# Kernel tuning notes

Measured on AMD Instinct MI355X. Metric: run time of the kernel, lower is better.

The kernel has to match this reference:

```python
import jax, jax.numpy as jnp
import numpy as np

K = 4  # kNN neighbors


def build_edges(density_maps, k):
    B, _, H, W = density_maps.shape
    N = H * W
    flat = density_maps.reshape(B, N)
    # [B, N, N] pairwise absolute density distance
    dist = jnp.abs(flat[:, :, None] - flat[:, None, :])
    # k nearest (excluding self at position 0)
    tgt = jnp.argsort(dist, axis=2)[:, :, 1:k + 1]  # [B, N, k]
    src = jnp.broadcast_to(jnp.arange(N)[None, :, None], (B, N, k))
    offset = (jnp.arange(B) * N)[:, None, None]
    src = (src + offset).reshape(-1)
    tgt = (tgt + offset).reshape(-1)
    n_total = B * N
    loops = jnp.arange(n_total)
    row = jnp.concatenate([src, loops])  # source nodes
    col = jnp.concatenate([tgt, loops])  # target nodes
    return row, col, n_total


def gcn_conv(x, row, col, W, b, n_nodes):
    # symmetric deg^-1/2 normalization, deg computed on target (col)
    deg = jax.ops.segment_sum(jnp.ones_like(col, dtype=x.dtype), col, num_segments=n_nodes)
    dinv = jnp.where(deg > 0, jax.lax.rsqrt(deg), 0.0)
    norm = dinv[row] * dinv[col]  # [E]
    h = x @ W  # transform first, then propagate
    msg = norm[:, None] * h[row]
    out = jax.ops.segment_sum(msg, col, num_segments=n_nodes)
    return out + b


def setup_inputs() -> dict:
    key = jax.random.key(0)
    k1, k2, k3, k4, k5, k6 = jax.random.split(key, 6)
    B, Cin, Chid, Cout, H, W = 4, 256, 512, 256, 64, 64
    density_maps = jax.random.uniform(k1, (B, 1, H, W), dtype=jnp.float32)
    feature_maps = jax.random.normal(k2, (B, Cin, H, W), dtype=jnp.float32)
    W1 = jax.random.normal(k3, (Cin, Chid), dtype=jnp.float32) * (1.0 / np.sqrt(Cin))
    b1 = jnp.zeros((Chid,), dtype=jnp.float32)
    W2 = jax.random.normal(k4, (Chid, Cout), dtype=jnp.float32) * (1.0 / np.sqrt(Chid))
    b2 = jnp.zeros((Cout,), dtype=jnp.float32)
    return {"density_maps": density_maps, "feature_maps": feature_maps,
            "W1": W1, "b1": b1, "W2": W2, "b2": b2}


def reference(density_maps, feature_maps, W1, b1, W2, b2):
    B, Cin, H, Wd = feature_maps.shape
    row, col, n_total = build_edges(density_maps, K)
    # [B,C,H,W] -> [B*H*W, C] node features
    x = feature_maps.transpose(0, 2, 3, 1).reshape(-1, Cin)
    h = jax.nn.relu(gcn_conv(x, row, col, W1, b1, n_total))
    out = jax.nn.relu(gcn_conv(h, row, col, W2, b2, n_total))
    return out.reshape(B, H, Wd, -1).transpose(0, 3, 1, 2)
```

## Files before the change

kernel.cpp:

```cpp
#include <hip/hip_runtime.h>
#include <hip/hip_bf16.h>
#include <stdint.h>

#define N_NODES 16384
#define NPB     4096
#define NB      4
#define KNN     4
#define WIN     12
#define NBUK    4096

typedef short bf16x8 __attribute__((ext_vector_type(8)));
typedef float f32x4 __attribute__((ext_vector_type(4)));
typedef unsigned short u16x8 __attribute__((ext_vector_type(8)));

__device__ __forceinline__ unsigned short f2bf(float f) {
  unsigned u = __float_as_uint(f);
  unsigned r = (u + 0x7fff + ((u >> 16) & 1)) >> 16;
  return (unsigned short)r;
}
__device__ __forceinline__ float bf2f(unsigned short u) {
  return __uint_as_float(((unsigned)u) << 16);
}

__global__ __launch_bounds__(1024)
void bucket_kernel(const float* __restrict__ dm,
                   unsigned long long* __restrict__ skeys_g,
                   int* __restrict__ rank_g,
                   int* __restrict__ deg) {
  __shared__ int sHist[4096];
  __shared__ int sCur[4096];
  __shared__ unsigned long long sKeys[4096];
  int* part1 = (int*)sKeys;
  int* part2 = (int*)(sKeys + 512);
  const int t = threadIdx.x, b = blockIdx.x;
  const float* d = dm + b * NPB;

  unsigned long long kv[4]; int bk[4];
#pragma unroll
  for (int r = 0; r < 4; ++r) {
    int i = t + r * 1024;
    sHist[i] = 0;
    deg[b * NPB + i] = 1;
  }
  __syncthreads();
#pragma unroll
  for (int r = 0; r < 4; ++r) {
    int i = t + r * 1024;
    float v = d[i];
    kv[r] = (((unsigned long long)__float_as_uint(v)) << 32) | (unsigned)i;
    int k = (int)(v * (float)NBUK); if (k > NBUK - 1) k = NBUK - 1;
    bk[r] = k;
    atomicAdd(&sHist[k], 1);
  }
  __syncthreads();
  int c0 = sHist[4 * t + 0], c1 = sHist[4 * t + 1];
  int c2 = sHist[4 * t + 2], c3 = sHist[4 * t + 3];
  part1[t] = c0 + c1 + c2 + c3;
  __syncthreads();
  if (t < 64) {
    int s = 0;
#pragma unroll
    for (int k = 0; k < 16; ++k) s += part1[16 * t + k];
    part2[t] = s;
  }
  __syncthreads();
  if (t == 0) {
    int a = 0;
    for (int u = 0; u < 64; ++u) { int v = part2[u]; part2[u] = a; a += v; }
  }
  __syncthreads();
  int base = part2[t >> 4];
  for (int k = (t >> 4) * 16; k < t; ++k) base += part1[k];
  sHist[4 * t + 0] = base; sCur[4 * t + 0] = base; base += c0;
  sHist[4 * t + 1] = base; sCur[4 * t + 1] = base; base += c1;
  sHist[4 * t + 2] = base; sCur[4 * t + 2] = base; base += c2;
  sHist[4 * t + 3] = base; sCur[4 * t + 3] = base;
  __syncthreads();
#pragma unroll
  for (int r = 0; r < 4; ++r) {
    int slot = atomicAdd(&sCur[bk[r]], 1);
    sKeys[slot] = kv[r];
  }
  __syncthreads();
#pragma unroll
  for (int r = 0; r < 4; ++r) {
    int g = t + r * 1024;
    int s0 = sHist[g];
    int s1 = (g == NPB - 1) ? NPB : sHist[g + 1];
    for (int i = s0 + 1; i < s1; ++i) {
      unsigned long long x = sKeys[i];
      int j = i - 1;
      while (j >= s0 && sKeys[j] > x) { sKeys[j + 1] = sKeys[j]; --j; }
      sKeys[j + 1] = x;
    }
  }
  __syncthreads();
#pragma unroll
  for (int r = 0; r < 4; ++r) {
    int i = t + r * 1024;
    unsigned long long k = sKeys[i];
    skeys_g[b * NPB + i] = k;
    rank_g[b * NPB + (int)(k & 0xffffffffull)] = i;
  }
}

__global__ void knn_select_kernel(const unsigned long long* __restrict__ skeys,
                                  int* __restrict__ tgt, int* __restrict__ deg) {
  int p = blockIdx.x * 256 + threadIdx.x;
  if (p >= N_NODES) return;
  int b = p >> 12, pl = p & (NPB - 1);
  const unsigned long long* sk = skeys + b * NPB;
  unsigned long long kp = sk[pl];
  float di = __uint_as_float((unsigned)(kp >> 32));
  int lo = pl - WIN; if (lo < 0) lo = 0;
  int hi = pl + WIN; if (hi > NPB - 1) hi = NPB - 1;
  unsigned long long k0 = ~0ull, k1 = ~0ull, k2 = ~0ull, k3 = ~0ull, k4 = ~0ull;
  for (int q = lo; q <= hi; ++q) {
    unsigned long long key = sk[q];
    float v = __uint_as_float((unsigned)(key >> 32));
    float dist = fabsf(di - v);
    unsigned long long dk = (((unsigned long long)__float_as_uint(dist)) << 24) |
                            ((key & 0xfffull) << 12) | (unsigned)q;
    if (dk < k4) {
      if (dk < k0)      { k4 = k3; k3 = k2; k2 = k1; k1 = k0; k0 = dk; }
      else if (dk < k1) { k4 = k3; k3 = k2; k2 = k1; k1 = dk; }
      else if (dk < k2) { k4 = k3; k3 = k2; k2 = dk; }
      else if (dk < k3) { k4 = k3; k3 = dk; }
      else              { k4 = dk; }
    }
  }
  int base = b * NPB;
  int t0 = base + (int)(k1 & 0xfff);
  int t1 = base + (int)(k2 & 0xfff);
  int t2 = base + (int)(k3 & 0xfff);
  int t3 = base + (int)(k4 & 0xfff);
  tgt[p * KNN + 0] = t0; atomicAdd(&deg[t0], 1);
  tgt[p * KNN + 1] = t1; atomicAdd(&deg[t1], 1);
  tgt[p * KNN + 2] = t2; atomicAdd(&deg[t2], 1);
  tgt[p * KNN + 3] = t3; atomicAdd(&deg[t3], 1);
}

__global__ void cvt_all_kernel(const float* __restrict__ fm, unsigned short* __restrict__ px0,
                               const float* __restrict__ W1, unsigned short* __restrict__ W1t,
                               const float* __restrict__ W2, unsigned short* __restrict__ W2t,
                               const int* __restrict__ rank) {
  __shared__ float tile[64][33];
  int z = blockIdx.z;
  const float* in; unsigned short* outbase; int Rin, Cin, r0, c0;
  bool perm = false;
  if (z < NB) {
    in = fm + (size_t)z * 256 * 4096; outbase = px0 + (size_t)z * NPB * 256;
    Rin = 256; Cin = 4096; perm = true;
    c0 = blockIdx.x * 32; r0 = blockIdx.y * 64;
  } else {
    int id = blockIdx.y * 128 + blockIdx.x;
    if (id < 64)       { in = W1; outbase = W1t; Rin = 256; Cin = 512; c0 = (id & 15) * 32; r0 = (id >> 4) * 64; }
    else if (id < 128) { id -= 64; in = W2; outbase = W2t; Rin = 512; Cin = 256; c0 = (id & 7) * 32; r0 = (id >> 3) * 64; }
    else return;
  }
  int tx = threadIdx.x & 31, ty = threadIdx.x >> 5;
  const float* ip = in + (size_t)(r0 + ty) * Cin + c0 + tx;
#pragma unroll
  for (int i = 0; i < 8; ++i) tile[ty + 8 * i][tx] = ip[(size_t)(8 * i) * Cin];
  __syncthreads();
  int orow = threadIdx.x >> 3;
  int oseg = (threadIdx.x & 7) * 8;
  int outrow = c0 + orow;
  if (perm) outrow = rank[(size_t)z * NPB + outrow];
  unsigned short* op = outbase + (size_t)outrow * Rin + r0 + oseg;
  u16x8 o;
#pragma unroll
  for (int k = 0; k < 8; ++k) o[k] = f2bf(tile[oseg + k][orow]);
  *(u16x8*)op = o;
}

__global__ void transpose_kernel(const float* __restrict__ in, float* __restrict__ out,
                                 int Rin, int Cin) {
  __shared__ float tile[32][33];
  int c0 = blockIdx.x * 32, r0 = blockIdx.y * 32, b = blockIdx.z;
  int tx = threadIdx.x & 31, ty = threadIdx.x >> 5;
  const float* ip = in + ((size_t)b * Rin + r0) * Cin + c0;
#pragma unroll
  for (int i = 0; i < 32; i += 8) tile[ty + i][tx] = ip[(size_t)(ty + i) * Cin + tx];
  __syncthreads();
  float* op = out + ((size_t)b * Cin + c0) * Rin + r0;
#pragma unroll
  for (int i = 0; i < 32; i += 8) op[(size_t)(ty + i) * Rin + tx] = tile[tx][ty + i];
}

__global__ void prop_kernel(const unsigned short* __restrict__ in,
                            unsigned short* __restrict__ out,
                            const int* __restrict__ tgt, const int* __restrict__ deg) {
  int i = blockIdx.x * 8 + (threadIdx.x >> 5);
  int l = threadIdx.x & 31;
  int b0 = i & ~(NPB - 1);
  int lo = i - WIN; if (lo < b0) lo = b0;
  int hi = i + WIN; if (hi > b0 + NPB - 1) hi = b0 + NPB - 1;
  float a[8] = {};
  for (int q = lo; q <= hi; ++q) {
    int4 tq = *(const int4*)(tgt + q * 4);
    int c = (q == i) + (tq.x == i) + (tq.y == i) + (tq.z == i) + (tq.w == i);
    if (c) {
      float dj = (float)c * rsqrtf((float)deg[q]);
      u16x8 u = *(const u16x8*)(in + (size_t)q * 256 + l * 8);
#pragma unroll
      for (int k = 0; k < 8; ++k) a[k] = fmaf(dj, bf2f(u[k]), a[k]);
    }
  }
  float di = rsqrtf((float)deg[i]);
  u16x8 o;
#pragma unroll
  for (int k = 0; k < 8; ++k) o[k] = f2bf(a[k] * di);
  *(u16x8*)(out + (size_t)i * 256 + l * 8) = o;
}

__global__ void prop2_kernel(const unsigned short* __restrict__ in,
                             float* __restrict__ out,
                             const int* __restrict__ tgt, const int* __restrict__ deg,
                             const float* __restrict__ bias,
                             const unsigned long long* __restrict__ skeys) {
  int i = blockIdx.x * 8 + (threadIdx.x >> 5);
  int l = threadIdx.x & 31;
  int b0 = i & ~(NPB - 1);
  int lo = i - WIN; if (lo < b0) lo = b0;
  int hi = i + WIN; if (hi > b0 + NPB - 1) hi = b0 + NPB - 1;
  float a[8] = {};
  for (int q = lo; q <= hi; ++q) {
    int4 tq = *(const int4*)(tgt + q * 4);
    int c = (q == i) + (tq.x == i) + (tq.y == i) + (tq.z == i) + (tq.w == i);
    if (c) {
      float dj = (float)c * rsqrtf((float)deg[q]);
      u16x8 u = *(const u16x8*)(in + (size_t)q * 256 + l * 8);
#pragma unroll
      for (int k = 0; k < 8; ++k) a[k] = fmaf(dj, bf2f(u[k]), a[k]);
    }
  }
  float di = rsqrtf((float)deg[i]);
  int node = b0 + (int)(skeys[i] & 0xffffffffull);
  float4 o0, o1;
  o0.x = fmaxf(a[0] * di + bias[l * 8 + 0], 0.f);
  o0.y = fmaxf(a[1] * di + bias[l * 8 + 1], 0.f);
  o0.z = fmaxf(a[2] * di + bias[l * 8 + 2], 0.f);
  o0.w = fmaxf(a[3] * di + bias[l * 8 + 3], 0.f);
  o1.x = fmaxf(a[4] * di + bias[l * 8 + 4], 0.f);
  o1.y = fmaxf(a[5] * di + bias[l * 8 + 5], 0.f);
  o1.z = fmaxf(a[6] * di + bias[l * 8 + 6], 0.f);
  o1.w = fmaxf(a[7] * di + bias[l * 8 + 7], 0.f);
  *(float4*)(out + (size_t)node * 256 + l * 8) = o0;
  *(float4*)(out + (size_t)node * 256 + l * 8 + 4) = o1;
}

template <bool BIAS_RELU, bool OUT_BF16, int NI>
__global__ __launch_bounds__(256)
void gemm_bf16_kernel(const unsigned short* __restrict__ A,
                      const unsigned short* __restrict__ Bt,
                      void* __restrict__ C, const float* __restrict__ bias,
                      int M, int N, int K) {
  __shared__ char lds[8192 + NI * 8192];
  const int tid = threadIdx.x;
  const int l = tid & 63, w = tid >> 6;
  const int bm = blockIdx.x * 64, bn = blockIdx.y * (64 * NI);
  f32x4 acc[4][NI] = {};

  for (int k0 = 0; k0 < K; k0 += 64) {
    __syncthreads();
#pragma unroll
    for (int q = 0; q < 2; ++q) {
      int o = q * 4096 + tid * 16;
      int r = o >> 7;
      int gc = ((o >> 4) & 7) ^ (r & 7);
      const char* srcA = (const char*)A + ((size_t)(bm + r) * K + k0) * 2 + gc * 16;
      __builtin_amdgcn_global_load_lds(
          (const __attribute__((address_space(1))) void*)srcA,
          (__attribute__((address_space(3))) void*)(lds + o), 16, 0, 0);
    }
#pragma unroll
    for (int q = 0; q < 2 * NI; ++q) {
      int o = q * 4096 + tid * 16;
      int r = o >> 7;
      int gc = ((o >> 4) & 7) ^ (r & 7);
      const char* srcB = (const char*)Bt + ((size_t)(bn + r) * K + k0) * 2 + gc * 16;
      __builtin_amdgcn_global_load_lds(
          (const __attribute__((address_space(1))) void*)srcB,
          (__attribute__((address_space(3))) void*)(lds + 8192 + o), 16, 0, 0);
    }
    __syncthreads();

#pragma unroll
    for (int kk = 0; kk < 64; kk += 32) {
      bf16x8 af[4], bf[NI];
      int gc = (kk >> 3) + (l >> 4);
#pragma unroll
      for (int mi = 0; mi < 4; ++mi) {
        int r = mi * 16 + (l & 15);
        af[mi] = *(const bf16x8*)(lds + r * 128 + ((gc ^ (r & 7)) << 4));
      }
#pragma unroll
      for (int ni = 0; ni < NI; ++ni) {
        int r = w * (16 * NI) + ni * 16 + (l & 15);
        bf[ni] = *(const bf16x8*)(lds + 8192 + r * 128 + ((gc ^ (r & 7)) << 4));
      }
#pragma unroll
      for (int mi = 0; mi < 4; ++mi)
#pragma unroll
        for (int ni = 0; ni < NI; ++ni)
          acc[mi][ni] = __builtin_amdgcn_mfma_f32_16x16x32_bf16(af[mi], bf[ni],
                                                                acc[mi][ni], 0, 0, 0);
    }
  }

#pragma unroll
  for (int mi = 0; mi < 4; ++mi) {
#pragma unroll
    for (int ni = 0; ni < NI; ++ni) {
      int row0 = bm + mi * 16 + ((l >> 4) << 2);
      int col = bn + w * (16 * NI) + ni * 16 + (l & 15);
      float bv = BIAS_RELU ? bias[col] : 0.f;
      f32x4 v = acc[mi][ni];
#pragma unroll
      for (int r = 0; r < 4; ++r) {
        float val = v[r];
        if (BIAS_RELU) val = fmaxf(val + bv, 0.f);
        if (OUT_BF16)
          ((unsigned short*)C)[(size_t)(row0 + r) * N + col] = f2bf(val);
        else
          ((float*)C)[(size_t)(row0 + r) * N + col] = val;
      }
    }
  }
}

extern "C" void kernel_launch(void* const* d_in, const int* in_sizes, int n_in,
                              void* d_out, int out_size, void* d_ws, size_t ws_size,
                              hipStream_t stream) {
  const float* dm = (const float*)d_in[0];
  const float* fm = (const float*)d_in[1];
  const float* W1 = (const float*)d_in[2];
  const float* b1 = (const float*)d_in[3];
  const float* W2 = (const float*)d_in[4];
  const float* b2 = (const float*)d_in[5];
  float* out = (float*)d_out;

  char* ws = (char*)d_ws;
  int*                tgt   = (int*)(ws + 0x000000);
  int*                deg   = (int*)(ws + 0x040000);
  unsigned long long* skeys = (unsigned long long*)(ws + 0x100000);
  int*                rank  = (int*)(ws + 0x130000);
  unsigned short*     W1t   = (unsigned short*)(ws + 0x190000);
  unsigned short*     W2t   = (unsigned short*)(ws + 0x1D0000);
  unsigned short*     px0   = (unsigned short*)(ws + 0x0400000);
  unsigned short*     px    = (unsigned short*)(ws + 0x0C00000);
  unsigned short*     h1    = (unsigned short*)(ws + 0x1400000);
  unsigned short*     t2    = (unsigned short*)(ws + 0x2400000);
  float*              xout  = (float*)(ws + 0x2C00000);
  (void)ws_size; (void)in_sizes; (void)n_in; (void)out_size;

  bucket_kernel<<<NB, 1024, 0, stream>>>(dm, skeys, rank, deg);
  knn_select_kernel<<<64, 256, 0, stream>>>(skeys, tgt, deg);

  cvt_all_kernel<<<dim3(128, 4, NB + 1), 256, 0, stream>>>(fm, px0, W1, W1t, W2, W2t, rank);

  prop_kernel<<<N_NODES / 8, 256, 0, stream>>>(px0, px, tgt, deg);
  gemm_bf16_kernel<true, true, 2><<<dim3(256, 4), 256, 0, stream>>>(
      px, W1t, h1, b1, 16384, 512, 256);

  gemm_bf16_kernel<false, true, 1><<<dim3(256, 4), 256, 0, stream>>>(
      h1, W2t, t2, nullptr, 16384, 256, 512);
  prop2_kernel<<<N_NODES / 8, 256, 0, stream>>>(t2, xout, tgt, deg, b2, skeys);

  transpose_kernel<<<dim3(8, 128, NB), 256, 0, stream>>>(xout, out, 4096, 256);
}
```

Baseline: 88.86 us.

## Fuse kNN selection into bucket kernel and encode in-edges as bitmask

The kNN selection now runs inside the bucket sort kernel, using the sorted keys already in shared memory. Degrees are accumulated with shared atomics, and incoming edges are recorded as a 25-bit per-node window mask, so a separate launch, global atomics and the tgt/deg buffers go away. The propagation kernels read the mask and precomputed dinv instead of scanning 25 neighbours' tgt entries and computing rsqrt each time. The first GEMM also switches to NI=1 with twice the grid in y. The cost is that the kNN work now runs on only 4 blocks rather than 64.

New measurement: 82.17 us. -7.5%, faster.

```diff
diff --git a/kernel.cpp b/kernel.cpp
--- a/kernel.cpp
+++ b/kernel.cpp
@@ -26,10 +26,12 @@
 void bucket_kernel(const float* __restrict__ dm,
                    unsigned long long* __restrict__ skeys_g,
                    int* __restrict__ rank_g,
-                   int* __restrict__ deg) {
+                   float* __restrict__ dinv_g,
+                   unsigned* __restrict__ mask_g) {
   __shared__ int sHist[4096];
   __shared__ int sCur[4096];
   __shared__ unsigned long long sKeys[4096];
+  __shared__ unsigned sMask[4096];
   int* part1 = (int*)sKeys;
   int* part2 = (int*)(sKeys + 512);
   const int t = threadIdx.x, b = blockIdx.x;
@@ -37,11 +39,7 @@
 
   unsigned long long kv[4]; int bk[4];
 #pragma unroll
-  for (int r = 0; r < 4; ++r) {
-    int i = t + r * 1024;
-    sHist[i] = 0;
-    deg[b * NPB + i] = 1;
-  }
+  for (int r = 0; r < 4; ++r) sHist[t + r * 1024] = 0;
   __syncthreads();
 #pragma unroll
   for (int r = 0; r < 4; ++r) {
@@ -98,46 +96,49 @@
 #pragma unroll
   for (int r = 0; r < 4; ++r) {
     int i = t + r * 1024;
+    sHist[i] = 1;
+    sMask[i] = 0;
+  }
+  __syncthreads();
+#pragma unroll
+  for (int r = 0; r < 4; ++r) {
+    int p = t + r * 1024;
+    unsigned long long kp = sKeys[p];
+    float di = __uint_as_float((unsigned)(kp >> 32));
+    int lo = p - WIN; if (lo < 0) lo = 0;
+    int hi = p + WIN; if (hi > NPB - 1) hi = NPB - 1;
+    unsigned long long k0 = ~0ull, k1 = ~0ull, k2 = ~0ull, k3 = ~0ull, k4 = ~0ull;
+    for (int q = lo; q <= hi; ++q) {
+      unsigned long long key = sKeys[q];
+      float v = __uint_as_float((unsigned)(key >> 32));
+      float dist = fabsf(di - v);
+      unsigned long long dk = (((unsigned long long)__float_as_uint(dist)) << 24) |
+                              ((key & 0xfffull) << 12) | (unsigned)q;
+      if (dk < k4) {
+        if (dk < k0)      { k4 = k3; k3 = k2; k2 = k1; k1 = k0; k0 = dk; }
+        else if (dk < k1) { k4 = k3; k3 = k2; k2 = k1; k1 = dk; }
+        else if (dk < k2) { k4 = k3; k3 = k2; k2 = dk; }
+        else if (dk < k3) { k4 = k3; k3 = dk; }
+        else              { k4 = dk; }
+      }
+    }
+    int t0 = (int)(k1 & 0xfff), t1 = (int)(k2 & 0xfff);
+    int t2 = (int)(k3 & 0xfff), t3 = (int)(k4 & 0xfff);
+    atomicAdd(&sHist[t0], 1); atomicOr(&sMask[t0], 1u << (p - t0 + WIN));
+    atomicAdd(&sHist[t1], 1); atomicOr(&sMask[t1], 1u << (p - t1 + WIN));
+    atomicAdd(&sHist[t2], 1); atomicOr(&sMask[t2], 1u << (p - t2 + WIN));
+    atomicAdd(&sHist[t3], 1); atomicOr(&sMask[t3], 1u << (p - t3 + WIN));
+  }
+  __syncthreads();
+#pragma unroll
+  for (int r = 0; r < 4; ++r) {
+    int i = t + r * 1024;
     unsigned long long k = sKeys[i];
     skeys_g[b * NPB + i] = k;
     rank_g[b * NPB + (int)(k & 0xffffffffull)] = i;
-  }
-}
-
-__global__ void knn_select_kernel(const unsigned long long* __restrict__ skeys,
-                                  int* __restrict__ tgt, int* __restrict__ deg) {
-  int p = blockIdx.x * 256 + threadIdx.x;
-  if (p >= N_NODES) return;
-  int b = p >> 12, pl = p & (NPB - 1);
-  const unsigned long long* sk = skeys + b * NPB;
-  unsigned long long kp = sk[pl];
-  float di = __uint_as_float((unsigned)(kp >> 32));
-  int lo = pl - WIN; if (lo < 0) lo = 0;
-  int hi = pl + WIN; if (hi > NPB - 1) hi = NPB - 1;
-  unsigned long long k0 = ~0ull, k1 = ~0ull, k2 = ~0ull, k3 = ~0ull, k4 = ~0ull;
-  for (int q = lo; q <= hi; ++q) {
-    unsigned long long key = sk[q];
-    float v = __uint_as_float((unsigned)(key >> 32));
-    float dist = fabsf(di - v);
-    unsigned long long dk = (((unsigned long long)__float_as_uint(dist)) << 24) |
-                            ((key & 0xfffull) << 12) | (unsigned)q;
-    if (dk < k4) {
-      if (dk < k0)      { k4 = k3; k3 = k2; k2 = k1; k1 = k0; k0 = dk; }
-      else if (dk < k1) { k4 = k3; k3 = k2; k2 = k1; k1 = dk; }
-      else if (dk < k2) { k4 = k3; k3 = k2; k2 = dk; }
-      else if (dk < k3) { k4 = k3; k3 = dk; }
-      else              { k4 = dk; }
-    }
-  }
-  int base = b * NPB;
-  int t0 = base + (int)(k1 & 0xfff);
-  int t1 = base + (int)(k2 & 0xfff);
-  int t2 = base + (int)(k3 & 0xfff);
-  int t3 = base + (int)(k4 & 0xfff);
-  tgt[p * KNN + 0] = t0; atomicAdd(&deg[t0], 1);
-  tgt[p * KNN + 1] = t1; atomicAdd(&deg[t1], 1);
-  tgt[p * KNN + 2] = t2; atomicAdd(&deg[t2], 1);
-  tgt[p * KNN + 3] = t3; atomicAdd(&deg[t3], 1);
+    dinv_g[b * NPB + i] = rsqrtf((float)sHist[i]);
+    mask_g[b * NPB + i] = sMask[i];
+  }
 }
 
 __global__ void cvt_all_kernel(const float* __restrict__ fm, unsigned short* __restrict__ px0,
@@ -190,24 +191,24 @@
 
 __global__ void prop_kernel(const unsigned short* __restrict__ in,
                             unsigned short* __restrict__ out,
-                            const int* __restrict__ tgt, const int* __restrict__ deg) {
+                            const unsigned* __restrict__ mask,
+                            const float* __restrict__ dinv) {
   int i = blockIdx.x * 8 + (threadIdx.x >> 5);
   int l = threadIdx.x & 31;
-  int b0 = i & ~(NPB - 1);
-  int lo = i - WIN; if (lo < b0) lo = b0;
-  int hi = i + WIN; if (hi > b0 + NPB - 1) hi = b0 + NPB - 1;
+  unsigned m = mask[i];
   float a[8] = {};
-  for (int q = lo; q <= hi; ++q) {
-    int4 tq = *(const int4*)(tgt + q * 4);
-    int c = (q == i) + (tq.x == i) + (tq.y == i) + (tq.z == i) + (tq.w == i);
+#pragma unroll
+  for (int off = 0; off < 2 * WIN + 1; ++off) {
+    int c = ((m >> off) & 1) + (off == WIN);
     if (c) {
-      float dj = (float)c * rsqrtf((float)deg[q]);
+      int q = i + off - WIN;
+      float dj = (float)c * dinv[q];
       u16x8 u = *(const u16x8*)(in + (size_t)q * 256 + l * 8);
 #pragma unroll
       for (int k = 0; k < 8; ++k) a[k] = fmaf(dj, bf2f(u[k]), a[k]);
     }
   }
-  float di = rsqrtf((float)deg[i]);
+  float di = dinv[i];
   u16x8 o;
 #pragma unroll
   for (int k = 0; k < 8; ++k) o[k] = f2bf(a[k] * di);
@@ -216,27 +217,27 @@
 
 __global__ void prop2_kernel(const unsigned short* __restrict__ in,
                              float* __restrict__ out,
-                             const int* __restrict__ tgt, const int* __restrict__ deg,
+                             const unsigned* __restrict__ mask,
+                             const float* __restrict__ dinv,
                              const float* __restrict__ bias,
                              const unsigned long long* __restrict__ skeys) {
   int i = blockIdx.x * 8 + (threadIdx.x >> 5);
   int l = threadIdx.x & 31;
-  int b0 = i & ~(NPB - 1);
-  int lo = i - WIN; if (lo < b0) lo = b0;
-  int hi = i + WIN; if (hi > b0 + NPB - 1) hi = b0 + NPB - 1;
+  unsigned m = mask[i];
   float a[8] = {};
-  for (int q = lo; q <= hi; ++q) {
-    int4 tq = *(const int4*)(tgt + q * 4);
-    int c = (q == i) + (tq.x == i) + (tq.y == i) + (tq.z == i) + (tq.w == i);
+#pragma unroll
+  for (int off = 0; off < 2 * WIN + 1; ++off) {
+    int c = ((m >> off) & 1) + (off == WIN);
     if (c) {
-      float dj = (float)c * rsqrtf((float)deg[q]);
+      int q = i + off - WIN;
+      float dj = (float)c * dinv[q];
       u16x8 u = *(const u16x8*)(in + (size_t)q * 256 + l * 8);
 #pragma unroll
       for (int k = 0; k < 8; ++k) a[k] = fmaf(dj, bf2f(u[k]), a[k]);
     }
   }
-  float di = rsqrtf((float)deg[i]);
-  int node = b0 + (int)(skeys[i] & 0xffffffffull);
+  float di = dinv[i];
+  int node = (i & ~(NPB - 1)) + (int)(skeys[i] & 0xffffffffull);
   float4 o0, o1;
   o0.x = fmaxf(a[0] * di + bias[l * 8 + 0], 0.f);
   o0.y = fmaxf(a[1] * di + bias[l * 8 + 1], 0.f);
@@ -342,8 +343,8 @@
   float* out = (float*)d_out;
 
   char* ws = (char*)d_ws;
-  int*                tgt   = (int*)(ws + 0x000000);
-  int*                deg   = (int*)(ws + 0x040000);
+  float*              dinv  = (float*)(ws + 0x050000);
+  unsigned*           mask  = (unsigned*)(ws + 0x060000);
   unsigned long long* skeys = (unsigned long long*)(ws + 0x100000);
   int*                rank  = (int*)(ws + 0x130000);
   unsigned short*     W1t   = (unsigned short*)(ws + 0x190000);
@@ -355,18 +356,17 @@
   float*              xout  = (float*)(ws + 0x2C00000);
   (void)ws_size; (void)in_sizes; (void)n_in; (void)out_size;
 
-  bucket_kernel<<<NB, 1024, 0, stream>>>(dm, skeys, rank, deg);
-  knn_select_kernel<<<64, 256, 0, stream>>>(skeys, tgt, deg);
+  bucket_kernel<<<NB, 1024, 0, stream>>>(dm, skeys, rank, dinv, mask);
 
   cvt_all_kernel<<<dim3(128, 4, NB + 1), 256, 0, stream>>>(fm, px0, W1, W1t, W2, W2t, rank);
 
-  prop_kernel<<<N_NODES / 8, 256, 0, stream>>>(px0, px, tgt, deg);
-  gemm_bf16_kernel<true, true, 2><<<dim3(256, 4), 256, 0, stream>>>(
+  prop_kernel<<<N_NODES / 8, 256, 0, stream>>>(px0, px, mask, dinv);
+  gemm_bf16_kernel<true, true, 1><<<dim3(256, 8), 256, 0, stream>>>(
       px, W1t, h1, b1, 16384, 512, 256);
 
   gemm_bf16_kernel<false, true, 1><<<dim3(256, 4), 256, 0, stream>>>(
       h1, W2t, t2, nullptr, 16384, 256, 512);
-  prop2_kernel<<<N_NODES / 8, 256, 0, stream>>>(t2, xout, tgt, deg, b2, skeys);
+  prop2_kernel<<<N_NODES / 8, 256, 0, stream>>>(t2, xout, mask, dinv, b2, skeys);
 
   transpose_kernel<<<dim3(8, 128, NB), 256, 0, stream>>>(xout, out, 4096, 256);
 }
```
